# Performance work log

Measured on AMD Instinct MI355X. Metric: run time of the kernel, lower is better.

## Reference

```python
import jax, jax.numpy as jnp
import numpy as np
import math


def _instance_cl(z1, z2):
    # z1, z2: [B, T, C] -> per-element instance contrastive loss [B, T]
    B = z1.shape[0]
    z = jnp.concatenate([z1, z2], axis=0)          # [2B, T, C]
    z = z.transpose(1, 0, 2)                        # [T, 2B, C]
    sim = jnp.einsum('tic,tjc->tij', z, z)          # [T, 2B, 2B]
    # drop diagonal: tril(-1) shifted + triu(1) shifted -> [T, 2B, 2B-1]
    logits = jnp.tril(sim, -1)[:, :, :-1] + jnp.triu(sim, 1)[:, :, 1:]
    logits = -jax.nn.log_softmax(logits, axis=-1)
    i = jnp.arange(B)
    loss = (logits[:, i, B + i - 1] + logits[:, B + i, i]) / 2.0   # [T, B]
    return loss.T                                    # [B, T]


def _temporal_cl(z1, z2):
    # z1, z2: [B, T, C] -> per-timestep temporal contrastive loss [B, T]
    T = z1.shape[1]
    z = jnp.concatenate([z1, z2], axis=1)            # [B, 2T, C]
    sim = jnp.einsum('bic,bjc->bij', z, z)           # [B, 2T, 2T]
    logits = jnp.tril(sim, -1)[:, :, :-1] + jnp.triu(sim, 1)[:, :, 1:]
    logits = -jax.nn.log_softmax(logits, axis=-1)
    t = jnp.arange(T)
    return (logits[:, t, T + t - 1] + logits[:, T + t, t]) / 2.0   # [B, T]


def _contrastive_corr(z1, z2, alpha=0.5):
    # per-(batch, timestep) contrastive score, shape [B, L]
    return alpha * _instance_cl(z1, z2) + (1.0 - alpha) * _temporal_cl(z1, z2)


def setup_inputs() -> dict:
    key = jax.random.key(0)
    k1, k2, k3 = jax.random.split(key, 3)
    B, L, H, E = 4, 2048, 8, 64
    queries = jax.random.normal(k1, (B, L, H, E), dtype=jnp.float32)
    keys = jax.random.normal(k2, (B, L, H, E), dtype=jnp.float32)
    values = jax.random.normal(k3, (B, L, H, E), dtype=jnp.float32)
    attn_mask = jnp.zeros((1,), dtype=bool)  # unused; ProbMask is rebuilt internally
    return {"queries": queries, "keys": keys, "values": values, "attn_mask": attn_mask}


FACTOR = 1.0


def reference(queries, keys, values, attn_mask):
    B, L, H, E = queries.shape
    # S == L here so key/value slicing branch is a no-op
    corr = _contrastive_corr(queries.reshape(B, L, H * E),
                             keys.reshape(B, L, H * E))       # [B, L]
    top_k = int(FACTOR * math.log(L))                          # static (=7 for L=2048)
    _, index = jax.lax.top_k(corr.mean(axis=0), top_k)         # [K]
    corr_top = corr[:, index]                                  # [B, K]
    # scores[b,h,k,l] = corr_top[b,k] broadcast over h and l
    scores = jnp.broadcast_to(corr_top[:, None, :, None], (B, H, top_k, L))
    # ProbMask: mask future positions l > index[k] (causal for the selected queries)
    mask = jnp.arange(L)[None, :] > index[:, None]             # [K, L]
    scores = jnp.where(mask[None, None, :, :], -jnp.inf, scores)
    attn = jax.nn.softmax(scores, axis=-1)                     # [B, H, K, L]
    V = values.transpose(0, 2, 1, 3)                           # [B, H, L, D]
    context = jnp.cumsum(V, axis=2)                            # initial context (mask_flag=True)
    out = jnp.einsum('bhkl,bhld->bhkd', attn, V)               # [B, H, K, D]
    context = context.at[:, :, index, :].set(out)              # scatter update
    return context
```

## Files before the change

kernel.cpp:

```cpp
#include <hip/hip_runtime.h>
#include <math.h>


typedef __attribute__((ext_vector_type(8))) short short8;
typedef __attribute__((ext_vector_type(8))) unsigned short ushort8;
typedef __attribute__((ext_vector_type(4))) float f32x4;

typedef const __attribute__((address_space(1))) void* gas_ptr;
typedef __attribute__((address_space(3))) void* las_ptr;

#define EXP_OFF 80.0f

__device__ __forceinline__ void async_cp16(const void* g, void* l) {
  __builtin_amdgcn_global_load_lds((gas_ptr)g, (las_ptr)l, 16, 0, 0);
}

__device__ __forceinline__ unsigned short f2bf(float x) {
  union { float f; unsigned int u; } v; v.f = x;
  unsigned int r = v.u + 0x7FFFu + ((v.u >> 16) & 1u);
  return (unsigned short)(r >> 16);
}

__global__ __launch_bounds__(256) void convert_bf16_kernel(
    const float* __restrict__ Q, const float* __restrict__ K,
    unsigned short* __restrict__ Z) {
  int tid = blockIdx.x * 256 + threadIdx.x;
  int row = tid >> 6;
  int c0 = (tid & 63) * 8;
  int b = row >> 12, i = row & 4095;
  const float* src = (i < 2048)
      ? Q + ((size_t)(b * 2048 + i) * 512 + c0)
      : K + ((size_t)(b * 2048 + (i - 2048)) * 512 + c0);
  float4 v0 = ((const float4*)src)[0];
  float4 v1 = ((const float4*)src)[1];
  ushort8 o;
  o[0] = f2bf(v0.x); o[1] = f2bf(v0.y); o[2] = f2bf(v0.z); o[3] = f2bf(v0.w);
  o[4] = f2bf(v1.x); o[5] = f2bf(v1.y); o[6] = f2bf(v1.z); o[7] = f2bf(v1.w);
  *(ushort8*)(Z + (size_t)row * 512 + c0) = o;
}

__global__ __launch_bounds__(256, 3) void temporal_gemm_kernel(
    const unsigned short* __restrict__ Z, float* __restrict__ part) {
  int id = blockIdx.x;
  int x = id & 7;
  int b = x >> 1;
  int t = (id >> 3) * 2 + (x & 1);
  int cj = (int)((sqrtf(8.0f * (float)t + 1.0f) - 1.0f) * 0.5f);
  while ((cj + 1) * (cj + 2) / 2 <= t) cj++;
  while (cj * (cj + 1) / 2 > t) cj--;
  int ri = t - cj * (cj + 1) / 2;
  const unsigned short* Zb = Z + (size_t)b * 4096 * 512;

  __shared__ __align__(16) unsigned short As[2][128 * 32];
  __shared__ __align__(16) unsigned short Bs[2][128 * 32];

  int tid = threadIdx.x;
  int w = tid >> 6, lane = tid & 63;
  int wr = w >> 1, wc = w & 1;
  int lm = lane & 15, q = lane >> 4;
  int swz = q ^ ((lm >> 1) & 3);

  int srow = lane >> 2;
  int kq = (lane & 3) ^ ((lane >> 3) & 3);
  int rl0 = w * 16 + srow;
  int rl1 = 64 + rl0;
  const unsigned short* gA0 = Zb + (size_t)(ri * 128 + rl0) * 512 + kq * 8;
  const unsigned short* gA1 = Zb + (size_t)(ri * 128 + rl1) * 512 + kq * 8;
  const unsigned short* gB0 = Zb + (size_t)(cj * 128 + rl0) * 512 + kq * 8;
  const unsigned short* gB1 = Zb + (size_t)(cj * 128 + rl1) * 512 + kq * 8;
  int lo0 = (w * 16) * 32;
  int lo1 = (64 + w * 16) * 32;

  f32x4 acc[4][4];
#pragma unroll
  for (int mi = 0; mi < 4; mi++)
#pragma unroll
    for (int ni = 0; ni < 4; ni++) acc[mi][ni] = (f32x4)(0.f);

  async_cp16(gA0, As[0] + lo0);
  async_cp16(gA1, As[0] + lo1);
  async_cp16(gB0, Bs[0] + lo0);
  async_cp16(gB1, Bs[0] + lo1);

  for (int kc = 0; kc < 16; ++kc) {
    int cur = kc & 1;
    __syncthreads();

    if (kc < 15) {
      int go = (kc + 1) * 32;
      async_cp16(gA0 + go, As[cur ^ 1] + lo0);
      async_cp16(gA1 + go, As[cur ^ 1] + lo1);
      async_cp16(gB0 + go, Bs[cur ^ 1] + lo0);
      async_cp16(gB1 + go, Bs[cur ^ 1] + lo1);
    }

    short8 af[4], bfr[4];
#pragma unroll
    for (int mi = 0; mi < 4; mi++) {
      int ar = wr * 64 + mi * 16 + lm;
      af[mi] = *(const short8*)(As[cur] + ar * 32 + swz * 8);
    }
#pragma unroll
    for (int ni = 0; ni < 4; ni++) {
      int bc = wc * 64 + ni * 16 + lm;
      bfr[ni] = *(const short8*)(Bs[cur] + bc * 32 + swz * 8);
    }
#pragma unroll
    for (int mi = 0; mi < 4; mi++)
#pragma unroll
      for (int ni = 0; ni < 4; ni++)
        acc[mi][ni] = __builtin_amdgcn_mfma_f32_16x16x32_bf16(
            af[mi], bfr[ni], acc[mi][ni], 0, 0, 0);
  }

  float rsum[4][4];
  float csum[4];
#pragma unroll
  for (int mi = 0; mi < 4; mi++)
#pragma unroll
    for (int rr = 0; rr < 4; rr++) rsum[mi][rr] = 0.f;
#pragma unroll
  for (int ni = 0; ni < 4; ni++) csum[ni] = 0.f;

#pragma unroll
  for (int mi = 0; mi < 4; mi++) {
#pragma unroll
    for (int ni = 0; ni < 4; ni++) {
#pragma unroll
      for (int rr = 0; rr < 4; rr++) {
        int R = ri * 128 + wr * 64 + mi * 16 + q * 4 + rr;
        int Cg = cj * 128 + wc * 64 + ni * 16 + lm;
        float e = (R != Cg) ? __expf(acc[mi][ni][rr] - EXP_OFF) : 0.f;
        rsum[mi][rr] += e;
        csum[ni] += e;
      }
    }
  }

#pragma unroll
  for (int mi = 0; mi < 4; mi++) {
#pragma unroll
    for (int rr = 0; rr < 4; rr++) {
      float s = rsum[mi][rr];
      s += __shfl_xor(s, 1);
      s += __shfl_xor(s, 2);
      s += __shfl_xor(s, 4);
      s += __shfl_xor(s, 8);
      if (lm == 0) {
        int R = ri * 128 + wr * 64 + mi * 16 + q * 4 + rr;
        part[((size_t)(b * 4096 + R)) * 64 + cj * 2 + wc] = s;
      }
    }
  }

  if (ri != cj) {
#pragma unroll
    for (int ni = 0; ni < 4; ni++) {
      float s = csum[ni];
      s += __shfl_xor(s, 16);
      s += __shfl_xor(s, 32);
      if (q == 0) {
        int Cg = cj * 128 + wc * 64 + ni * 16 + lm;
        part[((size_t)(b * 4096 + Cg)) * 64 + ri * 2 + wr] = s;
      }
    }
  }
}

__global__ __launch_bounds__(256) void merge_row_kernel(
    const float* __restrict__ part, float* __restrict__ lse_temp) {
  int row = blockIdx.x * 256 + threadIdx.x;
  const float4* p = (const float4*)(part + (size_t)row * 64);
  float s = 0.f;
#pragma unroll
  for (int i = 0; i < 16; i++) {
    float4 v = p[i];
    s += v.x + v.y + v.z + v.w;
  }
  lse_temp[row] = EXP_OFF + __logf(s);
}

__global__ __launch_bounds__(256) void instance_kernel(
    const unsigned short* __restrict__ Z,
    float* __restrict__ lse_inst ,
    float* __restrict__ posdot ) {
  int wave = (blockIdx.x * 256 + threadIdx.x) >> 6;
  int t0 = wave * 2;
  int lane = threadIdx.x & 63;
  int lm = lane & 15, q = lane >> 4;
  int tt = (lm < 8) ? t0 : t0 + 1;
  int v = lm & 7;
  size_t zrow = (v < 4) ? ((size_t)v * 4096 + tt)
                        : ((size_t)(v - 4) * 4096 + 2048 + tt);
  const unsigned short* g = Z + zrow * 512 + q * 8;

  f32x4 acc0 = (f32x4)(0.f), acc1 = (f32x4)(0.f);
#pragma unroll
  for (int kc = 0; kc < 16; kc += 2) {
    short8 a0 = *(const short8*)(g + kc * 32);
    short8 a1 = *(const short8*)(g + kc * 32 + 32);
    acc0 = __builtin_amdgcn_mfma_f32_16x16x32_bf16(a0, a0, acc0, 0, 0, 0);
    acc1 = __builtin_amdgcn_mfma_f32_16x16x32_bf16(a1, a1, acc1, 0, 0, 0);
  }
  f32x4 acc = acc0 + acc1;

#pragma unroll
  for (int rr = 0; rr < 4; rr++) {
    int i = q * 4 + rr;
    float val = acc[rr];
    bool samehalf = ((i < 8) == (lm < 8));
    int t = (i < 8) ? t0 : t0 + 1;
    int iv = i & 7;
    if (samehalf && iv < 4 && (lm & 7) == iv + 4)
      posdot[iv * 2048 + t] = val;
    float dd = (samehalf && lm != i) ? val : -INFINITY;
    float mt = dd;
    mt = fmaxf(mt, __shfl_xor(mt, 1));
    mt = fmaxf(mt, __shfl_xor(mt, 2));
    mt = fmaxf(mt, __shfl_xor(mt, 4));
    float e = __expf(dd - mt);
    e += __shfl_xor(e, 1);
    e += __shfl_xor(e, 2);
    e += __shfl_xor(e, 4);
    if ((lm & 7) == 0 && samehalf) lse_inst[t * 8 + iv] = mt + __logf(e);
  }
}

__global__ __launch_bounds__(256) void combine_topk_kernel(
    const float* __restrict__ lse_inst, const float* __restrict__ lse_temp,
    const float* __restrict__ posdot, int* __restrict__ index_out) {
  __shared__ float wmax[4];
  __shared__ int widx[4];
  int tid = threadIdx.x;
  int base = tid * 8;
  float v[8];
#pragma unroll
  for (int r = 0; r < 8; r++) {
    int t = base + r;
    float sum = 0.f;
#pragma unroll
    for (int b = 0; b < 4; b++) {
      sum += 0.25f * (lse_inst[t * 8 + b] + lse_inst[t * 8 + 4 + b] +
                      lse_temp[b * 4096 + t] + lse_temp[b * 4096 + 2048 + t]) -
             posdot[b * 2048 + t];
    }
    v[r] = sum * 0.25f;
  }
  int lane = tid & 63, w = tid >> 6;
  for (int k = 0; k < 7; k++) {
    float bv = v[0];
    int bi = base;
#pragma unroll
    for (int r = 1; r < 8; r++)
      if (v[r] > bv) { bv = v[r]; bi = base + r; }
#pragma unroll
    for (int d = 1; d < 64; d <<= 1) {
      float ov = __shfl_xor(bv, d);
      int oi = __shfl_xor(bi, d);
      if (ov > bv || (ov == bv && oi < bi)) { bv = ov; bi = oi; }
    }
    if (lane == 0) { wmax[w] = bv; widx[w] = bi; }
    __syncthreads();
    float BV = wmax[0];
    int BI = widx[0];
#pragma unroll
    for (int ww = 1; ww < 4; ww++)
      if (wmax[ww] > BV || (wmax[ww] == BV && widx[ww] < BI)) {
        BV = wmax[ww];
        BI = widx[ww];
      }
    if (tid == 0) index_out[k] = BI;
    if (BI >= base && BI < base + 8) v[BI - base] = -INFINITY;
    __syncthreads();
  }
}

__global__ __launch_bounds__(64) void cumsum_psum_kernel(
    const float* __restrict__ V, float* __restrict__ psum) {
  int gb = blockIdx.x;
  int bh = gb >> 6, g = gb & 63;
  int h = bh & 7, b = bh >> 3;
  int lane = threadIdx.x;
  int ro = lane >> 4, e4 = (lane & 15) * 4;
  const float* base =
      V + (size_t)(b * 2048 + g * 32 + ro) * 512 + h * 64 + e4;
  float sx = 0.f, sy = 0.f, sz = 0.f, sw = 0.f;
#pragma unroll
  for (int k = 0; k < 8; k++) {
    float4 v = *(const float4*)(base + (size_t)(k * 4) * 512);
    sx += v.x; sy += v.y; sz += v.z; sw += v.w;
  }
  sx += __shfl_xor(sx, 16); sy += __shfl_xor(sy, 16);
  sz += __shfl_xor(sz, 16); sw += __shfl_xor(sw, 16);
  sx += __shfl_xor(sx, 32); sy += __shfl_xor(sy, 32);
  sz += __shfl_xor(sz, 32); sw += __shfl_xor(sw, 32);
  if (ro == 0) {
    float4 o = {sx, sy, sz, sw};
    *(float4*)(psum + ((size_t)bh * 64 + g) * 64 + e4) = o;
  }
}

__global__ __launch_bounds__(256) void cumsum_write_kernel(
    const float* __restrict__ V, const float* __restrict__ psum,
    const int* __restrict__ index, float* __restrict__ out) {
  int blk = blockIdx.x;
  int bh = blk >> 4, chunk = blk & 15;
  int h = bh & 7, b = bh >> 3;
  int tid = threadIdx.x;
  int e = tid & 63, sub = tid >> 6;
  int g = chunk * 4 + sub;

  const float* ps = psum + (size_t)bh * 64 * 64;
  float run = 0.f;
  for (int gg = 0; gg < g; ++gg) run += ps[gg * 64 + e];

  int idx[7];
#pragma unroll
  for (int k = 0; k < 7; k++) idx[k] = index[k];

  const float* Vbase = V + (size_t)(b * 2048) * 512 + h * 64 + e;
  float* obase = out + (size_t)bh * 2048 * 64 + e;

  int l0 = g * 32;
#pragma unroll 4
  for (int l = l0; l < l0 + 32; ++l) {
    run += Vbase[(size_t)l * 512];
    float o = run;
    bool special = false;
#pragma unroll
    for (int k = 0; k < 7; k++) special = special || (idx[k] == l);
    if (special) o = run / (float)(l + 1);
    obase[(size_t)l * 64] = o;
  }
}

extern "C" void kernel_launch(void* const* d_in, const int* in_sizes, int n_in,
                              void* d_out, int out_size, void* d_ws, size_t ws_size,
                              hipStream_t stream) {
  const float* Q = (const float*)d_in[0];
  const float* K = (const float*)d_in[1];
  const float* V = (const float*)d_in[2];
  float* out = (float*)d_out;

  unsigned short* Z = (unsigned short*)d_ws;
  float* base = (float*)d_ws + 4 * 4096 * 512 / 2;
  float* part = base;
  float* lse_t = base + 4 * 4096 * 64;
  float* lse_i = lse_t + 16384;
  float* posd = lse_i + 16384;
  int* idx = (int*)(posd + 8192);
  float* psum = part;

  convert_bf16_kernel<<<4096, 256, 0, stream>>>(Q, K, Z);
  temporal_gemm_kernel<<<4 * 528, 256, 0, stream>>>(Z, part);
  instance_kernel<<<256, 256, 0, stream>>>(Z, lse_i, posd);
  merge_row_kernel<<<64, 256, 0, stream>>>(part, lse_t);
  combine_topk_kernel<<<1, 256, 0, stream>>>(lse_i, lse_t, posd, idx);
  cumsum_psum_kernel<<<2048, 64, 0, stream>>>(V, psum);
  cumsum_write_kernel<<<512, 256, 0, stream>>>(V, psum, idx, out);
}
```

Baseline: 193.5 us.

## Enlarge temporal GEMM tiles to 256x256 with a 4-stage async LDS pipeline

Moves the temporal similarity GEMM from 128x128 tiles with 256 threads to 256x256 tiles with 512 threads. Staging uses 128 KB of dynamic LDS in a 4-deep global_load_lds pipeline with explicit vmcnt waits, and MFMA sections run at raised priority. Larger tiles cut repeated global and LDS loads of Z and the number of blocks. Because the new partial-sum slot layout leaves some slots unwritten, the partial-sum buffer is zeroed inside the convert kernel. In exchange there are fewer blocks (544) and lower occupancy per CU.

```diff
diff --git a/kernel.cpp b/kernel.cpp
--- a/kernel.cpp
+++ b/kernel.cpp
@@ -23,8 +23,9 @@
 
 __global__ __launch_bounds__(256) void convert_bf16_kernel(
     const float* __restrict__ Q, const float* __restrict__ K,
-    unsigned short* __restrict__ Z) {
+    unsigned short* __restrict__ Z, float* __restrict__ part) {
   int tid = blockIdx.x * 256 + threadIdx.x;
+  part[tid] = 0.f;
   int row = tid >> 6;
   int c0 = (tid & 63) * 8;
   int b = row >> 12, i = row & 4095;
@@ -39,8 +40,9 @@
   *(ushort8*)(Z + (size_t)row * 512 + c0) = o;
 }
 
-__global__ __launch_bounds__(256, 3) void temporal_gemm_kernel(
+__global__ __launch_bounds__(512) void temporal_gemm_kernel(
     const unsigned short* __restrict__ Z, float* __restrict__ part) {
+  extern __shared__ __align__(16) unsigned short smem[];
   int id = blockIdx.x;
   int x = id & 7;
   int b = x >> 1;
@@ -51,104 +53,109 @@
   int ri = t - cj * (cj + 1) / 2;
   const unsigned short* Zb = Z + (size_t)b * 4096 * 512;
 
-  __shared__ __align__(16) unsigned short As[2][128 * 32];
-  __shared__ __align__(16) unsigned short Bs[2][128 * 32];
-
   int tid = threadIdx.x;
   int w = tid >> 6, lane = tid & 63;
-  int wr = w >> 1, wc = w & 1;
+  int wr = w >> 2, wc = w & 3;
   int lm = lane & 15, q = lane >> 4;
   int swz = q ^ ((lm >> 1) & 3);
 
-  int srow = lane >> 2;
+  int srow = w * 16 + (lane >> 2);
   int kq = (lane & 3) ^ ((lane >> 3) & 3);
-  int rl0 = w * 16 + srow;
-  int rl1 = 64 + rl0;
-  const unsigned short* gA0 = Zb + (size_t)(ri * 128 + rl0) * 512 + kq * 8;
-  const unsigned short* gA1 = Zb + (size_t)(ri * 128 + rl1) * 512 + kq * 8;
-  const unsigned short* gB0 = Zb + (size_t)(cj * 128 + rl0) * 512 + kq * 8;
-  const unsigned short* gB1 = Zb + (size_t)(cj * 128 + rl1) * 512 + kq * 8;
+  const unsigned short* gA0 = Zb + (size_t)(ri * 256 + srow) * 512 + kq * 8;
+  const unsigned short* gA1 = gA0 + (size_t)128 * 512;
+  const unsigned short* gB0 = Zb + (size_t)(cj * 256 + srow) * 512 + kq * 8;
+  const unsigned short* gB1 = gB0 + (size_t)128 * 512;
   int lo0 = (w * 16) * 32;
-  int lo1 = (64 + w * 16) * 32;
-
-  f32x4 acc[4][4];
-#pragma unroll
-  for (int mi = 0; mi < 4; mi++)
+  int lo1 = (128 + w * 16) * 32;
+
+  f32x4 acc[8][4];
+#pragma unroll
+  for (int mi = 0; mi < 8; mi++)
 #pragma unroll
     for (int ni = 0; ni < 4; ni++) acc[mi][ni] = (f32x4)(0.f);
 
-  async_cp16(gA0, As[0] + lo0);
-  async_cp16(gA1, As[0] + lo1);
-  async_cp16(gB0, Bs[0] + lo0);
-  async_cp16(gB1, Bs[0] + lo1);
-
-  for (int kc = 0; kc < 16; ++kc) {
-    int cur = kc & 1;
-    __syncthreads();
-
-    if (kc < 15) {
-      int go = (kc + 1) * 32;
-      async_cp16(gA0 + go, As[cur ^ 1] + lo0);
-      async_cp16(gA1 + go, As[cur ^ 1] + lo1);
-      async_cp16(gB0 + go, Bs[cur ^ 1] + lo0);
-      async_cp16(gB1 + go, Bs[cur ^ 1] + lo1);
-    }
-
-    short8 af[4], bfr[4];
-#pragma unroll
-    for (int mi = 0; mi < 4; mi++) {
-      int ar = wr * 64 + mi * 16 + lm;
-      af[mi] = *(const short8*)(As[cur] + ar * 32 + swz * 8);
+#define STAGE(kt_)                                                     \
+  do {                                                                 \
+    unsigned short* base_ = smem + (((kt_) & 3) * 16384);              \
+    int go_ = (kt_) * 32;                                              \
+    async_cp16(gA0 + go_, base_ + lo0);                                \
+    async_cp16(gA1 + go_, base_ + lo1);                                \
+    async_cp16(gB0 + go_, base_ + 8192 + lo0);                         \
+    async_cp16(gB1 + go_, base_ + 8192 + lo1);                         \
+  } while (0)
+
+  STAGE(0);
+  STAGE(1);
+  STAGE(2);
+
+  for (int kt = 0; kt < 16; ++kt) {
+    if (kt + 3 < 16) STAGE(kt + 3);
+
+    if (kt < 13)
+      asm volatile("s_waitcnt vmcnt(12)" ::: "memory");
+    else if (kt == 13)
+      asm volatile("s_waitcnt vmcnt(8)" ::: "memory");
+    else if (kt == 14)
+      asm volatile("s_waitcnt vmcnt(4)" ::: "memory");
+    else
+      asm volatile("s_waitcnt vmcnt(0)" ::: "memory");
+    asm volatile("s_barrier" ::: "memory");
+
+    const unsigned short* A = smem + (kt & 3) * 16384;
+    const unsigned short* B = A + 8192;
+    short8 af[8], bfr[4];
+#pragma unroll
+    for (int mi = 0; mi < 8; mi++) {
+      int ar = wr * 128 + mi * 16 + lm;
+      af[mi] = *(const short8*)(A + ar * 32 + swz * 8);
     }
 #pragma unroll
     for (int ni = 0; ni < 4; ni++) {
       int bc = wc * 64 + ni * 16 + lm;
-      bfr[ni] = *(const short8*)(Bs[cur] + bc * 32 + swz * 8);
-    }
-#pragma unroll
-    for (int mi = 0; mi < 4; mi++)
+      bfr[ni] = *(const short8*)(B + bc * 32 + swz * 8);
+    }
+    __builtin_amdgcn_s_setprio(1);
+#pragma unroll
+    for (int mi = 0; mi < 8; mi++)
 #pragma unroll
       for (int ni = 0; ni < 4; ni++)
         acc[mi][ni] = __builtin_amdgcn_mfma_f32_16x16x32_bf16(
             af[mi], bfr[ni], acc[mi][ni], 0, 0, 0);
-  }
-
-  float rsum[4][4];
+    __builtin_amdgcn_s_setprio(0);
+    asm volatile("s_barrier" ::: "memory");
+  }
+#undef STAGE
+
   float csum[4];
 #pragma unroll
-  for (int mi = 0; mi < 4; mi++)
-#pragma unroll
-    for (int rr = 0; rr < 4; rr++) rsum[mi][rr] = 0.f;
-#pragma unroll
   for (int ni = 0; ni < 4; ni++) csum[ni] = 0.f;
 
 #pragma unroll
-  for (int mi = 0; mi < 4; mi++) {
+  for (int mi = 0; mi < 8; mi++) {
+    float rs[4];
+#pragma unroll
+    for (int rr = 0; rr < 4; rr++) rs[rr] = 0.f;
 #pragma unroll
     for (int ni = 0; ni < 4; ni++) {
 #pragma unroll
       for (int rr = 0; rr < 4; rr++) {
-        int R = ri * 128 + wr * 64 + mi * 16 + q * 4 + rr;
-        int Cg = cj * 128 + wc * 64 + ni * 16 + lm;
+        int R = ri * 256 + wr * 128 + mi * 16 + q * 4 + rr;
+        int Cg = cj * 256 + wc * 64 + ni * 16 + lm;
         float e = (R != Cg) ? __expf(acc[mi][ni][rr] - EXP_OFF) : 0.f;
-        rsum[mi][rr] += e;
+        rs[rr] += e;
         csum[ni] += e;
       }
     }
-  }
-
-#pragma unroll
-  for (int mi = 0; mi < 4; mi++) {
 #pragma unroll
     for (int rr = 0; rr < 4; rr++) {
-      float s = rsum[mi][rr];
+      float s = rs[rr];
       s += __shfl_xor(s, 1);
       s += __shfl_xor(s, 2);
       s += __shfl_xor(s, 4);
       s += __shfl_xor(s, 8);
       if (lm == 0) {
-        int R = ri * 128 + wr * 64 + mi * 16 + q * 4 + rr;
-        part[((size_t)(b * 4096 + R)) * 64 + cj * 2 + wc] = s;
+        int R = ri * 256 + wr * 128 + mi * 16 + q * 4 + rr;
+        part[((size_t)(b * 4096 + R)) * 64 + cj * 4 + wc] = s;
       }
     }
   }
@@ -160,7 +167,7 @@
       s += __shfl_xor(s, 16);
       s += __shfl_xor(s, 32);
       if (q == 0) {
-        int Cg = cj * 128 + wc * 64 + ni * 16 + lm;
+        int Cg = cj * 256 + wc * 64 + ni * 16 + lm;
         part[((size_t)(b * 4096 + Cg)) * 64 + ri * 2 + wr] = s;
       }
     }
@@ -351,8 +358,15 @@
   int* idx = (int*)(posd + 8192);
   float* psum = part;
 
-  convert_bf16_kernel<<<4096, 256, 0, stream>>>(Q, K, Z);
-  temporal_gemm_kernel<<<4 * 528, 256, 0, stream>>>(Z, part);
+  static bool attr_set = false;
+  if (!attr_set) {
+    hipFuncSetAttribute((const void*)temporal_gemm_kernel,
+                        hipFuncAttributeMaxDynamicSharedMemorySize, 131072);
+    attr_set = true;
+  }
+
+  convert_bf16_kernel<<<4096, 256, 0, stream>>>(Q, K, Z, part);
+  temporal_gemm_kernel<<<544, 512, 131072, stream>>>(Z, part);
   instance_kernel<<<256, 256, 0, stream>>>(Z, lse_i, posd);
   merge_row_kernel<<<64, 256, 0, stream>>>(part, lse_t);
   combine_topk_kernel<<<1, 256, 0, stream>>>(lse_i, lse_t, posd, idx);
```

Result: slower. 207.6 us (+7.3%).
